# Kernel optimization log

Measured on AMD Instinct MI355X. Metric: run time of the kernel, lower is better.

## Reference

```python
import jax, jax.numpy as jnp
import numpy as np

D_MODEL = 1024
NUM_HEADS = 16
HEAD_DIM = D_MODEL // NUM_HEADS


def setup_inputs() -> dict:
    key = jax.random.key(0)
    k1, k2, k3 = jax.random.split(key, 3)
    B, S = 4, 2048
    x = jax.random.normal(k1, (B, S, D_MODEL), dtype=jnp.float32)
    # Linear weights; scale like torch's default-ish init for numerical sanity.
    w_qkv = jax.random.normal(k2, (D_MODEL, 3 * D_MODEL), dtype=jnp.float32) / np.sqrt(D_MODEL)
    b_qkv = jnp.zeros((3 * D_MODEL,), dtype=jnp.float32)
    w_out = jax.random.normal(k3, (D_MODEL, D_MODEL), dtype=jnp.float32) / np.sqrt(D_MODEL)
    b_out = jnp.zeros((D_MODEL,), dtype=jnp.float32)
    return {"x": x, "w_qkv": w_qkv, "b_qkv": b_qkv, "w_out": w_out, "b_out": b_out}


def reference(x, w_qkv, b_qkv, w_out, b_out):
    B, S, D = x.shape
    H, Hd = NUM_HEADS, HEAD_DIM
    # fused QKV projection, then chunk along last dim (same as torch.chunk)
    qkv = x @ w_qkv + b_qkv                       # [B, S, 3D]
    q, k, v = jnp.split(qkv, 3, axis=-1)          # each [B, S, D]
    q = q.reshape(B, S, H, Hd).transpose(0, 2, 1, 3)  # [B, H, S, Hd]
    k = k.reshape(B, S, H, Hd).transpose(0, 2, 1, 3)
    v = v.reshape(B, S, H, Hd).transpose(0, 2, 1, 3)
    scale = 1.0 / np.sqrt(Hd).astype(np.float32)
    scores = jnp.einsum('bhqd,bhkd->bhqk', q, k) * scale  # [B, H, S, S]
    attn = jax.nn.softmax(scores, axis=-1)
    out = jnp.einsum('bhqk,bhkd->bhqd', attn, v)           # [B, H, S, Hd]
    out = out.transpose(0, 2, 1, 3).reshape(B, S, D)
    return out @ w_out + b_out
```

## Files before the change

kernel.cpp:

```cpp
#include <hip/hip_runtime.h>
#include <stdint.h>

typedef unsigned short u16;
typedef __attribute__((ext_vector_type(8))) short   short8;
typedef __attribute__((ext_vector_type(8))) u16     ushort8;
typedef __attribute__((ext_vector_type(4))) float   f32x4;
typedef __attribute__((ext_vector_type(16))) float  f32x16;
typedef __attribute__((ext_vector_type(4))) unsigned int u32x4;

#define SEQ   2048
#define NH    16
#define HD    64
#define DM    1024
#define ROWS  8192
#define BHN   64

__device__ __forceinline__ u16 f2bf(float f){
  union { float f; uint32_t u; } v; v.f = f;
  return (u16)((v.u + 0x7fffu + ((v.u >> 16) & 1u)) >> 16);
}

__device__ __forceinline__ unsigned cvtpk(float a, float b){
  unsigned r;
  asm("v_cvt_pk_bf16_f32 %0, %1, %2" : "=v"(r) : "v"(a), "v"(b));
  return r;
}

__device__ __forceinline__ void pswap(unsigned &a, unsigned &b){
  asm volatile("v_permlane32_swap_b32 %0, %1" : "+v"(a), "+v"(b));
}

__device__ __forceinline__ float fexp2(float x){
  return __builtin_amdgcn_exp2f(x);
}

__device__ __forceinline__ float tsum16(const f32x16& s){
  float a0=s[0]+s[1], a1=s[2]+s[3], a2=s[4]+s[5], a3=s[6]+s[7];
  float a4=s[8]+s[9], a5=s[10]+s[11], a6=s[12]+s[13], a7=s[14]+s[15];
  float b0=a0+a1, b1=a2+a3, b2=a4+a5, b3=a6+a7;
  return (b0+b1)+(b2+b3);
}

#define GAS(p) ((const __attribute__((address_space(1))) void*)(p))
#define LAS(p) ((__attribute__((address_space(3))) void*)(p))

__global__ void conv_bf16_kernel(const float* __restrict__ in, u16* __restrict__ out, int n8){
  int i = blockIdx.x * blockDim.x + threadIdx.x;
  if (i >= n8) return;
  const float4* p = (const float4*)in + (size_t)i * 2;
  float4 a = p[0], b = p[1];
  ushort8 o;
  o[0]=f2bf(a.x); o[1]=f2bf(a.y); o[2]=f2bf(a.z); o[3]=f2bf(a.w);
  o[4]=f2bf(b.x); o[5]=f2bf(b.y); o[6]=f2bf(b.z); o[7]=f2bf(b.w);
  *(ushort8*)(out + (size_t)i * 8) = o;
}

__global__ void transpose_conv_kernel(const float* __restrict__ in, u16* __restrict__ out,
                                      int R, int C){
  __shared__ float tile[32][33];
  int c0 = blockIdx.x * 32, r0 = blockIdx.y * 32;
  int tx = threadIdx.x & 31, ty = threadIdx.x >> 5;
  #pragma unroll
  for (int i = 0; i < 4; i++)
    tile[ty + 8*i][tx] = in[(size_t)(r0 + ty + 8*i) * C + c0 + tx];
  __syncthreads();
  #pragma unroll
  for (int i = 0; i < 4; i++)
    out[(size_t)(c0 + ty + 8*i) * R + r0 + tx] = f2bf(tile[tx][ty + 8*i]);
}

#define BM 128
#define BN 128
#define BK 64

template<int MODE>
__global__ __launch_bounds__(256, 2) void gemm_kernel(
    const u16* __restrict__ A, const u16* __restrict__ Bt, const float* __restrict__ bias,
    u16* __restrict__ Qo, u16* __restrict__ Ko, u16* __restrict__ Vto,
    float* __restrict__ Cout)
{
  __shared__ __align__(16) u16 As[BM * BK];
  __shared__ __align__(16) u16 Bs[BN * BK];
  const int tid  = threadIdx.x;
  const int lane = tid & 63, wv = tid >> 6;
  const int wr = wv >> 1, wc = wv & 1;
  const int m0 = blockIdx.y * BM, n0 = blockIdx.x * BN;
  const int K = 1024;

  f32x4 acc[4][4] = {};

  for (int k0 = 0; k0 < K; k0 += BK) {
    #pragma unroll
    for (int i = 0; i < 4; i++) {
      int f = (i * 256 + tid) * 16;
      int row = f >> 7, inrow = f & 127;
      int src = inrow ^ ((row & 7) << 4);
      const u16* ga = A  + (size_t)(m0 + row) * K + k0 + (src >> 1);
      __builtin_amdgcn_global_load_lds(GAS(ga), LAS((char*)As + (i*256 + (wv<<6))*16), 16, 0, 0);
      const u16* gb = Bt + (size_t)(n0 + row) * K + k0 + (src >> 1);
      __builtin_amdgcn_global_load_lds(GAS(gb), LAS((char*)Bs + (i*256 + (wv<<6))*16), 16, 0, 0);
    }
    __syncthreads();
    #pragma unroll
    for (int kk = 0; kk < 2; kk++) {
      short8 af[4], bfr[4];
      #pragma unroll
      for (int i = 0; i < 4; i++) {
        int row = wr*64 + i*16 + (lane & 15);
        int kb  = (kk*64 + 16*(lane >> 4)) ^ ((row & 7) << 4);
        af[i] = *(const short8*)((const char*)As + row*128 + kb);
      }
      #pragma unroll
      for (int j = 0; j < 4; j++) {
        int row = wc*64 + j*16 + (lane & 15);
        int kb  = (kk*64 + 16*(lane >> 4)) ^ ((row & 7) << 4);
        bfr[j] = *(const short8*)((const char*)Bs + row*128 + kb);
      }
      #pragma unroll
      for (int i = 0; i < 4; i++)
        #pragma unroll
        for (int j = 0; j < 4; j++)
          acc[i][j] = __builtin_amdgcn_mfma_f32_16x16x32_bf16(af[i], bfr[j], acc[i][j], 0, 0, 0);
    }
    __syncthreads();
  }

  if (MODE == 0) {
    const int part = n0 >> 10;
    #pragma unroll
    for (int i = 0; i < 4; i++) {
      int row = m0 + wr*64 + i*16 + ((lane >> 4) << 2);
      int b = row >> 11, s = row & 2047;
      #pragma unroll
      for (int j = 0; j < 4; j++) {
        int col = n0 + wc*64 + j*16 + (lane & 15);
        int cn = col & 1023, h = cn >> 6, d = cn & 63;
        int bh = b * NH + h;
        #pragma unroll
        for (int r = 0; r < 4; r++) {
          float v = acc[i][j][r] + bias[col];
          int ss = s + r;
          if (part == 0)      Qo [((size_t)bh*SEQ + ss)*HD + d] = f2bf(v * 0.18033688011f);
          else if (part == 1) Ko [((size_t)bh*SEQ + ss)*HD + d] = f2bf(v);
          else                Vto[((size_t)bh*HD  + d)*SEQ + ss] = f2bf(v);
        }
      }
    }
  } else {
    #pragma unroll
    for (int i = 0; i < 4; i++) {
      int row = m0 + wr*64 + i*16 + ((lane >> 4) << 2);
      #pragma unroll
      for (int j = 0; j < 4; j++) {
        int col = n0 + wc*64 + j*16 + (lane & 15);
        float bv = bias[col];
        #pragma unroll
        for (int r = 0; r < 4; r++)
          Cout[(size_t)(row + r) * DM + col] = acc[i][j][r] + bv;
      }
    }
  }
}

#define STAGE(LOFF, T) do { \
    _Pragma("unroll") \
    for (int _i = 0; _i < 2; _i++) { \
      int _row = _i * 32 + (tid >> 3); \
      int _src = (((tid & 7) << 4) ^ ((_row & 7) << 4)) >> 1; \
      const u16* _gk = Kg + (((size_t)bh * SEQ + (T) * 64 + _row) << 6) + _src; \
      __builtin_amdgcn_global_load_lds(GAS(_gk), LAS(lds + (LOFF) + _i * 4096 + (wv << 10)), 16, 0, 0); \
      const u16* _gv = Vt + ((size_t)(bh * 64 + _row)) * SEQ + (T) * 64 + _src; \
      __builtin_amdgcn_global_load_lds(GAS(_gv), LAS(lds + (LOFF) + 8192 + _i * 4096 + (wv << 10)), 16, 0, 0); \
    } \
  } while (0)

#define WAITBAR() do { \
    asm volatile("s_waitcnt vmcnt(0) lgkmcnt(0)" ::: "memory"); \
    __builtin_amdgcn_s_barrier(); \
  } while (0)

#define PACK_PA(S, PA0, PA1) do { \
    unsigned a0 = cvtpk((S)[0],  (S)[1]),  b0 = cvtpk((S)[4],  (S)[5]); \
    unsigned a1 = cvtpk((S)[2],  (S)[3]),  b1 = cvtpk((S)[6],  (S)[7]); \
    unsigned a2 = cvtpk((S)[8],  (S)[9]),  b2 = cvtpk((S)[12], (S)[13]); \
    unsigned a3 = cvtpk((S)[10], (S)[11]), b3 = cvtpk((S)[14], (S)[15]); \
    pswap(a0, b0); pswap(a1, b1); pswap(a2, b2); pswap(a3, b3); \
    (PA0).u = (u32x4){a0, a1, b0, b1}; \
    (PA1).u = (u32x4){a2, a3, b2, b3}; \
  } while (0)

#define TILE64(BOFF) do { \
    _Pragma("unroll") \
    for (int H = 0; H < 2; H++) { \
      short8 kf[4]; \
      _Pragma("unroll") \
      for (int kd = 0; kd < 4; kd++) \
        kf[kd] = *(const short8*)(lds + (BOFF) + (32*H + l31) * 128 + ((32*kd + 16*hi) ^ swz)); \
      f32x16 sA, sB; \
      _Pragma("unroll") for (int i = 0; i < 16; i++) { sA[i] = -16.f; sB[i] = -16.f; } \
      __builtin_amdgcn_s_setprio(1); \
      _Pragma("unroll") \
      for (int kd = 0; kd < 4; kd++) { \
        sA = __builtin_amdgcn_mfma_f32_32x32x16_bf16(kf[kd], qfA[kd], sA, 0, 0, 0); \
        sB = __builtin_amdgcn_mfma_f32_32x32x16_bf16(kf[kd], qfB[kd], sB, 0, 0, 0); \
      } \
      __builtin_amdgcn_s_setprio(0); \
      _Pragma("unroll") for (int i = 0; i < 16; i++) { sA[i] = fexp2(sA[i]); sB[i] = fexp2(sB[i]); } \
      lpA += tsum16(sA); lpB += tsum16(sB); \
      union { u32x4 u; short8 s8; } paA0, paA1, paB0, paB1; \
      PACK_PA(sA, paA0, paA1); \
      PACK_PA(sB, paB0, paB1); \
      __builtin_amdgcn_s_setprio(1); \
      _Pragma("unroll") \
      for (int ki = 0; ki < 2; ki++) { \
        int vo = (64*H + 32*ki + 16*hi) ^ swz; \
        short8 vb0 = *(const short8*)(lds + (BOFF) + 8192  + l31 * 128 + vo); \
        short8 vb1 = *(const short8*)(lds + (BOFF) + 12288 + l31 * 128 + vo); \
        const short8 pA = ki ? paA1.s8 : paA0.s8; \
        const short8 pB = ki ? paB1.s8 : paB0.s8; \
        oA0 = __builtin_amdgcn_mfma_f32_32x32x16_bf16(pA, vb0, oA0, 0, 0, 0); \
        oA1 = __builtin_amdgcn_mfma_f32_32x32x16_bf16(pA, vb1, oA1, 0, 0, 0); \
        oB0 = __builtin_amdgcn_mfma_f32_32x32x16_bf16(pB, vb0, oB0, 0, 0, 0); \
        oB1 = __builtin_amdgcn_mfma_f32_32x32x16_bf16(pB, vb1, oB1, 0, 0, 0); \
      } \
      __builtin_amdgcn_s_setprio(0); \
    } \
  } while (0)

__global__ __launch_bounds__(256, 2) void attn_kernel(
    const u16* __restrict__ Q, const u16* __restrict__ Kg,
    const u16* __restrict__ Vt, u16* __restrict__ O)
{
  __shared__ __align__(16) char lds[32768];
  const int tid = threadIdx.x, lane = tid & 63, wv = tid >> 6;
  const int l31 = lane & 31, hi = lane >> 5;
  const int swz = (lane & 7) << 4;

  int flat = blockIdx.x;
  int nid = (flat & 7) * 64 + (flat >> 3);
  int bh = nid >> 3;
  int q0 = (nid & 7) * 256;

  short8 qfA[4], qfB[4];
  {
    int qrow = q0 + wv * 64 + l31;
    const u16* qp = Q + (((size_t)bh * SEQ + qrow) << 6) + hi * 8;
    #pragma unroll
    for (int kd = 0; kd < 4; kd++) {
      qfA[kd] = *(const short8*)(qp + kd * 16);
      qfB[kd] = *(const short8*)(qp + 2048 + kd * 16);
    }
  }

  f32x16 oA0 = {}, oA1 = {}, oB0 = {}, oB1 = {};
  float lpA = 0.f, lpB = 0.f;

  STAGE(0, 0);
  WAITBAR();
  for (int t = 0; t < 32; t += 2) {
    STAGE(16384, t + 1);
    TILE64(0);
    WAITBAR();
    if (t + 2 < 32) STAGE(0, t + 2);
    TILE64(16384);
    WAITBAR();
  }

  float lfA = lpA + __shfl_xor(lpA, 32);
  float lfB = lpB + __shfl_xor(lpB, 32);
  int b = bh >> 4, h = bh & 15;
  int qbase = q0 + wv * 64;
  #pragma unroll
  for (int r = 0; r < 16; r++) {
    int qrow = (r & 3) + 8 * (r >> 2) + 4 * hi;
    float invA = 1.0f / __shfl(lfA, qrow);
    float invB = 1.0f / __shfl(lfB, qrow);
    size_t rowA = ((size_t)(b * SEQ + qbase + qrow) << 10) + h * 64 + l31;
    size_t rowB = rowA + (32u << 10);
    O[rowA]      = f2bf(oA0[r] * invA);
    O[rowA + 32] = f2bf(oA1[r] * invA);
    O[rowB]      = f2bf(oB0[r] * invB);
    O[rowB + 32] = f2bf(oB1[r] * invB);
  }
}

extern "C" void kernel_launch(void* const* d_in, const int* in_sizes, int n_in,
                              void* d_out, int out_size, void* d_ws, size_t ws_size,
                              hipStream_t stream)
{
  const float* x     = (const float*)d_in[0];
  const float* w_qkv = (const float*)d_in[1];
  const float* b_qkv = (const float*)d_in[2];
  const float* w_out = (const float*)d_in[3];
  const float* b_out = (const float*)d_in[4];
  float* out = (float*)d_out;

  char* w = (char*)d_ws;
  u16* xb    = (u16*)(w);
  u16* wqkvT = (u16*)(w + 16777216);
  u16* woutT = (u16*)(w + 23068672);
  u16* Qw    = (u16*)(w + 25165824);
  u16* Kw    = (u16*)(w + 41943040);
  u16* Vtw   = (u16*)(w + 58720256);
  u16* Ow    = (u16*)(w + 75497472);

  conv_bf16_kernel<<<dim3(4096), dim3(256), 0, stream>>>(x, xb, ROWS * DM / 8);
  transpose_conv_kernel<<<dim3(96, 32), dim3(256), 0, stream>>>(w_qkv, wqkvT, 1024, 3072);
  transpose_conv_kernel<<<dim3(32, 32), dim3(256), 0, stream>>>(w_out, woutT, 1024, 1024);

  gemm_kernel<0><<<dim3(24, 64), dim3(256), 0, stream>>>(xb, wqkvT, b_qkv, Qw, Kw, Vtw, nullptr);
  attn_kernel<<<dim3(512), dim3(256), 0, stream>>>(Qw, Kw, Vtw, Ow);
  gemm_kernel<1><<<dim3(8, 64), dim3(256), 0, stream>>>(Ow, woutT, b_out, nullptr, nullptr, nullptr, out);
}
```

Before: 194.8 us.

## Replace QKV projection GEMM with 256x256 double-buffered 8-wave pipelined kernel

Adds a new QKV projection GEMM that uses 256x256 tiles, 8 waves per block and 128KB of double-buffered LDS. Async global-to-LDS loads of later K tiles are interleaved with MFMA sub-blocks, with partial vmcnt waits, s_setprio around the MFMAs, and an XCD-aware block remapping. The aim is better data reuse and hiding of load latency in the largest GEMM. The cost is heavy LDS use that limits occupancy, many barriers, and a more fragile hand-written schedule. The output projection GEMM is de-templated and otherwise unchanged.

```diff
diff --git a/kernel.cpp b/kernel.cpp
--- a/kernel.cpp
+++ b/kernel.cpp
@@ -43,6 +43,10 @@
 
 #define GAS(p) ((const __attribute__((address_space(1))) void*)(p))
 #define LAS(p) ((__attribute__((address_space(3))) void*)(p))
+
+#define BAR()   asm volatile("s_barrier" ::: "memory")
+#define BARV6() asm volatile("s_waitcnt vmcnt(6)\n\ts_barrier" ::: "memory")
+#define BARV0() asm volatile("s_waitcnt vmcnt(0)\n\ts_barrier" ::: "memory")
 
 __global__ void conv_bf16_kernel(const float* __restrict__ in, u16* __restrict__ out, int n8){
   int i = blockIdx.x * blockDim.x + threadIdx.x;
@@ -69,14 +73,146 @@
     out[(size_t)(c0 + ty + 8*i) * R + r0 + tx] = f2bf(tile[tx][ty + 8*i]);
 }
 
+__global__ __launch_bounds__(512, 2) void gemm8_kernel(
+    const u16* __restrict__ A, const u16* __restrict__ Bt, const float* __restrict__ bias,
+    u16* __restrict__ Qo, u16* __restrict__ Ko, u16* __restrict__ Vto)
+{
+  __shared__ __align__(16) char lds[131072];
+  const int tid = threadIdx.x, lane = tid & 63, wv = tid >> 6;
+  const int wm = wv >> 2, wn = wv & 3;
+  const int l15 = lane & 15, l4 = lane >> 4;
+
+  int bid = blockIdx.x;
+  int nid = (bid & 7) * 48 + (bid >> 3);
+  int tm = nid / 12, tn = nid - tm * 12;
+  const int m0 = tm * 256, n0 = tn * 256;
+
+  f32x4 acc[8][4] = {};
+
+  #define STG(REGION, SRC, ROW0, KT) do { \
+    _Pragma("unroll") \
+    for (int _u = 0; _u < 2; _u++) { \
+      int _r = _u*64 + (tid >> 3); \
+      int _sb = ((((tid & 7) << 4) ^ ((_r & 7) << 4)) >> 1); \
+      const u16* _g = (SRC) + (((size_t)((ROW0) + _r)) << 10) + ((KT) << 6) + _sb; \
+      __builtin_amdgcn_global_load_lds(GAS(_g), LAS(lds + (REGION) + _u*8192 + (wv << 10)), 16, 0, 0); \
+    } \
+  } while (0)
+
+  STG(0,              A,  m0,       0);
+  STG(16384,          A,  m0 + 128, 0);
+  STG(32768,          Bt, n0,       0);
+  STG(49152,          Bt, n0 + 128, 0);
+  STG(65536 + 49152,  Bt, n0 + 128, 1);
+  STG(65536 + 32768,  Bt, n0,       1);
+  STG(65536 + 16384,  A,  m0 + 128, 1);
+  BARV6();
+
+  short8 Af[4][2], Bf[2][2][2];
+
+  #define LD_A(BUF, M) do { \
+    _Pragma("unroll") for (int mr = 0; mr < 4; mr++) \
+      _Pragma("unroll") for (int kk = 0; kk < 2; kk++) { \
+        int row = (M)*64 + mr*16 + l15; \
+        Af[mr][kk] = *(const short8*)(lds + (BUF)*65536 + wm*16384 + row*128 \
+                       + ((kk*64 + 16*l4) ^ ((row & 7) << 4))); \
+      } \
+  } while (0)
+
+  #define LD_B(BUF, N) do { \
+    _Pragma("unroll") for (int jr = 0; jr < 2; jr++) \
+      _Pragma("unroll") for (int kk = 0; kk < 2; kk++) { \
+        int row = (wn & 1)*64 + (N)*32 + jr*16 + l15; \
+        Bf[N][jr][kk] = *(const short8*)(lds + (BUF)*65536 + 32768 + (wn >> 1)*16384 + row*128 \
+                          + ((kk*64 + 16*l4) ^ ((row & 7) << 4))); \
+      } \
+  } while (0)
+
+  #define MM(M, N) do { \
+    __builtin_amdgcn_s_setprio(1); \
+    _Pragma("unroll") for (int mr = 0; mr < 4; mr++) \
+      _Pragma("unroll") for (int jr = 0; jr < 2; jr++) \
+        _Pragma("unroll") for (int kk = 0; kk < 2; kk++) \
+          acc[(M)*4 + mr][(N)*2 + jr] = __builtin_amdgcn_mfma_f32_16x16x32_bf16( \
+              Af[mr][kk], Bf[N][jr][kk], acc[(M)*4 + mr][(N)*2 + jr], 0, 0, 0); \
+    __builtin_amdgcn_s_setprio(0); \
+  } while (0)
+
+  for (int i = 0; i < 7; i++) {
+    int t1 = 2*i + 1, t2 = 2*i + 2, t3 = 2*i + 3;
+    LD_A(0, 0); LD_B(0, 0);
+    STG(65536 + 0, A, m0, t1);
+    BAR();  MM(0, 0);  BAR();
+    LD_B(0, 1);
+    BAR();  MM(0, 1);  BAR();
+    LD_A(0, 1);
+    STG(32768, Bt, n0, t2);
+    STG(49152, Bt, n0 + 128, t2);
+    BAR();  MM(1, 1);  BAR();
+    STG(16384, A, m0 + 128, t2);
+    BAR();  MM(1, 0);  BARV6();
+    LD_A(1, 0); LD_B(1, 0);
+    STG(0, A, m0, t2);
+    BAR();  MM(0, 0);  BAR();
+    LD_B(1, 1);
+    BAR();  MM(0, 1);  BAR();
+    LD_A(1, 1);
+    STG(65536 + 32768, Bt, n0, t3);
+    STG(65536 + 49152, Bt, n0 + 128, t3);
+    BAR();  MM(1, 1);  BAR();
+    STG(65536 + 16384, A, m0 + 128, t3);
+    BAR();  MM(1, 0);  BARV6();
+  }
+
+  LD_A(0, 0); LD_B(0, 0);
+  STG(65536 + 0, A, m0, 15);
+  BAR();  MM(0, 0);  BAR();
+  LD_B(0, 1);
+  BAR();  MM(0, 1);  BAR();
+  LD_A(0, 1);
+  BAR();  MM(1, 1);  BAR();
+  BAR();  MM(1, 0);  BARV0();
+  LD_A(1, 0); LD_B(1, 0);
+  BAR();  MM(0, 0);  BAR();
+  LD_B(1, 1);
+  BAR();  MM(0, 1);  BAR();
+  LD_A(1, 1);
+  BAR();  MM(1, 1);  BAR();
+  MM(1, 0);
+
+  #undef STG
+  #undef LD_A
+  #undef LD_B
+  #undef MM
+
+  const int part = n0 >> 10;
+  #pragma unroll
+  for (int i = 0; i < 8; i++) {
+    int row = m0 + wm*128 + i*16 + (l4 << 2);
+    int b = row >> 11, s = row & 2047;
+    #pragma unroll
+    for (int j = 0; j < 4; j++) {
+      int col = n0 + wn*64 + j*16 + l15;
+      int cn = col & 1023, h = cn >> 6, d = cn & 63;
+      int bh = b * NH + h;
+      #pragma unroll
+      for (int r = 0; r < 4; r++) {
+        float v = acc[i][j][r] + bias[col];
+        int ss = s + r;
+        if (part == 0)      Qo [((size_t)bh*SEQ + ss)*HD + d] = f2bf(v * 0.18033688011f);
+        else if (part == 1) Ko [((size_t)bh*SEQ + ss)*HD + d] = f2bf(v);
+        else                Vto[((size_t)bh*HD  + d)*SEQ + ss] = f2bf(v);
+      }
+    }
+  }
+}
+
 #define BM 128
 #define BN 128
 #define BK 64
 
-template<int MODE>
 __global__ __launch_bounds__(256, 2) void gemm_kernel(
     const u16* __restrict__ A, const u16* __restrict__ Bt, const float* __restrict__ bias,
-    u16* __restrict__ Qo, u16* __restrict__ Ko, u16* __restrict__ Vto,
     float* __restrict__ Cout)
 {
   __shared__ __align__(16) u16 As[BM * BK];
@@ -125,39 +261,16 @@
     __syncthreads();
   }
 
-  if (MODE == 0) {
-    const int part = n0 >> 10;
+  #pragma unroll
+  for (int i = 0; i < 4; i++) {
+    int row = m0 + wr*64 + i*16 + ((lane >> 4) << 2);
     #pragma unroll
-    for (int i = 0; i < 4; i++) {
-      int row = m0 + wr*64 + i*16 + ((lane >> 4) << 2);
-      int b = row >> 11, s = row & 2047;
+    for (int j = 0; j < 4; j++) {
+      int col = n0 + wc*64 + j*16 + (lane & 15);
+      float bv = bias[col];
       #pragma unroll
-      for (int j = 0; j < 4; j++) {
-        int col = n0 + wc*64 + j*16 + (lane & 15);
-        int cn = col & 1023, h = cn >> 6, d = cn & 63;
-        int bh = b * NH + h;
-        #pragma unroll
-        for (int r = 0; r < 4; r++) {
-          float v = acc[i][j][r] + bias[col];
-          int ss = s + r;
-          if (part == 0)      Qo [((size_t)bh*SEQ + ss)*HD + d] = f2bf(v * 0.18033688011f);
-          else if (part == 1) Ko [((size_t)bh*SEQ + ss)*HD + d] = f2bf(v);
-          else                Vto[((size_t)bh*HD  + d)*SEQ + ss] = f2bf(v);
-        }
-      }
-    }
-  } else {
-    #pragma unroll
-    for (int i = 0; i < 4; i++) {
-      int row = m0 + wr*64 + i*16 + ((lane >> 4) << 2);
-      #pragma unroll
-      for (int j = 0; j < 4; j++) {
-        int col = n0 + wc*64 + j*16 + (lane & 15);
-        float bv = bias[col];
-        #pragma unroll
-        for (int r = 0; r < 4; r++)
-          Cout[(size_t)(row + r) * DM + col] = acc[i][j][r] + bv;
-      }
+      for (int r = 0; r < 4; r++)
+        Cout[(size_t)(row + r) * DM + col] = acc[i][j][r] + bv;
     }
   }
 }
@@ -175,8 +288,7 @@
   } while (0)
 
 #define WAITBAR() do { \
-    asm volatile("s_waitcnt vmcnt(0) lgkmcnt(0)" ::: "memory"); \
-    __builtin_amdgcn_s_barrier(); \
+    asm volatile("s_waitcnt vmcnt(0) lgkmcnt(0)\n\ts_barrier" ::: "memory"); \
   } while (0)
 
 #define PACK_PA(S, PA0, PA1) do { \
@@ -308,7 +420,7 @@
   transpose_conv_kernel<<<dim3(96, 32), dim3(256), 0, stream>>>(w_qkv, wqkvT, 1024, 3072);
   transpose_conv_kernel<<<dim3(32, 32), dim3(256), 0, stream>>>(w_out, woutT, 1024, 1024);
 
-  gemm_kernel<0><<<dim3(24, 64), dim3(256), 0, stream>>>(xb, wqkvT, b_qkv, Qw, Kw, Vtw, nullptr);
+  gemm8_kernel<<<dim3(384), dim3(512), 0, stream>>>(xb, wqkvT, b_qkv, Qw, Kw, Vtw);
   attn_kernel<<<dim3(512), dim3(256), 0, stream>>>(Qw, Kw, Vtw, Ow);
-  gemm_kernel<1><<<dim3(8, 64), dim3(256), 0, stream>>>(Ow, woutT, b_out, nullptr, nullptr, nullptr, out);
-}
+  gemm_kernel<<<dim3(8, 64), dim3(256), 0, stream>>>(Ow, woutT, b_out, out);
+}
```

New measurement: 203.4 us. +4.4%, slower.

## Halve attention query tile per block to double grid and occupancy

Applied to the files above, without the earlier changes.

The attention kernel now gives each wave 32 query rows instead of 64, so each block covers 128 queries and the grid grows from 512 to 1024 blocks. Launch bounds go from 2 to 4 blocks per CU, since the per-wave accumulator count halves. This is meant to fill the 256 CUs better and hide latency through higher occupancy. The cost is that every K/V tile is loaded into LDS twice as often per query, which doubles global and LDS traffic per unit of compute. The wait-and-barrier pair is also merged into a single inline asm block.

```diff
diff --git a/kernel.cpp b/kernel.cpp
--- a/kernel.cpp
+++ b/kernel.cpp
@@ -175,8 +175,7 @@
   } while (0)
 
 #define WAITBAR() do { \
-    asm volatile("s_waitcnt vmcnt(0) lgkmcnt(0)" ::: "memory"); \
-    __builtin_amdgcn_s_barrier(); \
+    asm volatile("s_waitcnt vmcnt(0) lgkmcnt(0)\n\ts_barrier" ::: "memory"); \
   } while (0)
 
 #define PACK_PA(S, PA0, PA1) do { \
@@ -196,38 +195,32 @@
       _Pragma("unroll") \
       for (int kd = 0; kd < 4; kd++) \
         kf[kd] = *(const short8*)(lds + (BOFF) + (32*H + l31) * 128 + ((32*kd + 16*hi) ^ swz)); \
-      f32x16 sA, sB; \
-      _Pragma("unroll") for (int i = 0; i < 16; i++) { sA[i] = -16.f; sB[i] = -16.f; } \
+      f32x16 s; \
+      _Pragma("unroll") for (int i = 0; i < 16; i++) s[i] = -16.f; \
       __builtin_amdgcn_s_setprio(1); \
       _Pragma("unroll") \
-      for (int kd = 0; kd < 4; kd++) { \
-        sA = __builtin_amdgcn_mfma_f32_32x32x16_bf16(kf[kd], qfA[kd], sA, 0, 0, 0); \
-        sB = __builtin_amdgcn_mfma_f32_32x32x16_bf16(kf[kd], qfB[kd], sB, 0, 0, 0); \
-      } \
+      for (int kd = 0; kd < 4; kd++) \
+        s = __builtin_amdgcn_mfma_f32_32x32x16_bf16(kf[kd], qf[kd], s, 0, 0, 0); \
       __builtin_amdgcn_s_setprio(0); \
-      _Pragma("unroll") for (int i = 0; i < 16; i++) { sA[i] = fexp2(sA[i]); sB[i] = fexp2(sB[i]); } \
-      lpA += tsum16(sA); lpB += tsum16(sB); \
-      union { u32x4 u; short8 s8; } paA0, paA1, paB0, paB1; \
-      PACK_PA(sA, paA0, paA1); \
-      PACK_PA(sB, paB0, paB1); \
+      _Pragma("unroll") for (int i = 0; i < 16; i++) s[i] = fexp2(s[i]); \
+      lp += tsum16(s); \
+      union { u32x4 u; short8 s8; } pa0, pa1; \
+      PACK_PA(s, pa0, pa1); \
       __builtin_amdgcn_s_setprio(1); \
       _Pragma("unroll") \
       for (int ki = 0; ki < 2; ki++) { \
         int vo = (64*H + 32*ki + 16*hi) ^ swz; \
-        short8 vb0 = *(const short8*)(lds + (BOFF) + 8192  + l31 * 128 + vo); \
-        short8 vb1 = *(const short8*)(lds + (BOFF) + 12288 + l31 * 128 + vo); \
-        const short8 pA = ki ? paA1.s8 : paA0.s8; \
-        const short8 pB = ki ? paB1.s8 : paB0.s8; \
-        oA0 = __builtin_amdgcn_mfma_f32_32x32x16_bf16(pA, vb0, oA0, 0, 0, 0); \
-        oA1 = __builtin_amdgcn_mfma_f32_32x32x16_bf16(pA, vb1, oA1, 0, 0, 0); \
-        oB0 = __builtin_amdgcn_mfma_f32_32x32x16_bf16(pB, vb0, oB0, 0, 0, 0); \
-        oB1 = __builtin_amdgcn_mfma_f32_32x32x16_bf16(pB, vb1, oB1, 0, 0, 0); \
+        short8 vb0 = *(const short8*)(lds + (BOFF) + 8192 + l31 * 128 + vo);             \
+        short8 vb1 = *(const short8*)(lds + (BOFF) + 8192 + (32 + l31) * 128 + vo);      \
+        const short8 pa = ki ? pa1.s8 : pa0.s8; \
+        oacc0 = __builtin_amdgcn_mfma_f32_32x32x16_bf16(pa, vb0, oacc0, 0, 0, 0); \
+        oacc1 = __builtin_amdgcn_mfma_f32_32x32x16_bf16(pa, vb1, oacc1, 0, 0, 0); \
       } \
       __builtin_amdgcn_s_setprio(0); \
     } \
   } while (0)
 
-__global__ __launch_bounds__(256, 2) void attn_kernel(
+__global__ __launch_bounds__(256, 4) void attn_kernel(
     const u16* __restrict__ Q, const u16* __restrict__ Kg,
     const u16* __restrict__ Vt, u16* __restrict__ O)
 {
@@ -237,23 +230,20 @@
   const int swz = (lane & 7) << 4;
 
   int flat = blockIdx.x;
-  int nid = (flat & 7) * 64 + (flat >> 3);
-  int bh = nid >> 3;
-  int q0 = (nid & 7) * 256;
-
-  short8 qfA[4], qfB[4];
+  int nid = (flat & 7) * 128 + (flat >> 3);
+  int bh = nid >> 4;
+  int q0 = (nid & 15) * 128;
+
+  short8 qf[4];
   {
-    int qrow = q0 + wv * 64 + l31;
+    int qrow = q0 + wv * 32 + l31;
     const u16* qp = Q + (((size_t)bh * SEQ + qrow) << 6) + hi * 8;
     #pragma unroll
-    for (int kd = 0; kd < 4; kd++) {
-      qfA[kd] = *(const short8*)(qp + kd * 16);
-      qfB[kd] = *(const short8*)(qp + 2048 + kd * 16);
-    }
-  }
-
-  f32x16 oA0 = {}, oA1 = {}, oB0 = {}, oB1 = {};
-  float lpA = 0.f, lpB = 0.f;
+    for (int kd = 0; kd < 4; kd++) qf[kd] = *(const short8*)(qp + kd * 16);
+  }
+
+  f32x16 oacc0 = {}, oacc1 = {};
+  float lp = 0.f;
 
   STAGE(0, 0);
   WAITBAR();
@@ -266,21 +256,16 @@
     WAITBAR();
   }
 
-  float lfA = lpA + __shfl_xor(lpA, 32);
-  float lfB = lpB + __shfl_xor(lpB, 32);
+  float lfull = lp + __shfl_xor(lp, 32);
   int b = bh >> 4, h = bh & 15;
-  int qbase = q0 + wv * 64;
+  int qbase = q0 + wv * 32;
   #pragma unroll
   for (int r = 0; r < 16; r++) {
     int qrow = (r & 3) + 8 * (r >> 2) + 4 * hi;
-    float invA = 1.0f / __shfl(lfA, qrow);
-    float invB = 1.0f / __shfl(lfB, qrow);
-    size_t rowA = ((size_t)(b * SEQ + qbase + qrow) << 10) + h * 64 + l31;
-    size_t rowB = rowA + (32u << 10);
-    O[rowA]      = f2bf(oA0[r] * invA);
-    O[rowA + 32] = f2bf(oA1[r] * invA);
-    O[rowB]      = f2bf(oB0[r] * invB);
-    O[rowB + 32] = f2bf(oB1[r] * invB);
+    float inv = 1.0f / __shfl(lfull, qrow);
+    size_t rowb = ((size_t)(b * SEQ + qbase + qrow) << 10) + h * 64 + l31;
+    O[rowb]      = f2bf(oacc0[r] * inv);
+    O[rowb + 32] = f2bf(oacc1[r] * inv);
   }
 }
 
@@ -309,6 +294,6 @@
   transpose_conv_kernel<<<dim3(32, 32), dim3(256), 0, stream>>>(w_out, woutT, 1024, 1024);
 
   gemm_kernel<0><<<dim3(24, 64), dim3(256), 0, stream>>>(xb, wqkvT, b_qkv, Qw, Kw, Vtw, nullptr);
-  attn_kernel<<<dim3(512), dim3(256), 0, stream>>>(Qw, Kw, Vtw, Ow);
+  attn_kernel<<<dim3(1024), dim3(256), 0, stream>>>(Qw, Kw, Vtw, Ow);
   gemm_kernel<1><<<dim3(8, 64), dim3(256), 0, stream>>>(Ow, woutT, b_out, nullptr, nullptr, nullptr, out);
 }
```

Result: slower. 391.3 us (+100.9%).

## Merge prep kernels into one launch and double attention K/V staging depth

Applied to the files above, without the earlier changes.

Merges the x conversion and the two weight transpose-convert kernels into a single prep_kernel that dispatches on block index, removing two launches. In attention, the LDS buffer grows to 64KB so each stage loads two 64-key tiles, and each barrier now covers two tiles of compute instead of one. This halves the barriers per KV sweep but doubles LDS per block, which can reduce occupancy and leaves more prefetch latency exposed per stage.

```diff
diff --git a/kernel.cpp b/kernel.cpp
--- a/kernel.cpp
+++ b/kernel.cpp
@@ -44,22 +44,27 @@
 #define GAS(p) ((const __attribute__((address_space(1))) void*)(p))
 #define LAS(p) ((__attribute__((address_space(3))) void*)(p))
 
-__global__ void conv_bf16_kernel(const float* __restrict__ in, u16* __restrict__ out, int n8){
-  int i = blockIdx.x * blockDim.x + threadIdx.x;
-  if (i >= n8) return;
-  const float4* p = (const float4*)in + (size_t)i * 2;
-  float4 a = p[0], b = p[1];
-  ushort8 o;
-  o[0]=f2bf(a.x); o[1]=f2bf(a.y); o[2]=f2bf(a.z); o[3]=f2bf(a.w);
-  o[4]=f2bf(b.x); o[5]=f2bf(b.y); o[6]=f2bf(b.z); o[7]=f2bf(b.w);
-  *(ushort8*)(out + (size_t)i * 8) = o;
-}
-
-__global__ void transpose_conv_kernel(const float* __restrict__ in, u16* __restrict__ out,
-                                      int R, int C){
+__global__ void prep_kernel(const float* __restrict__ x, u16* __restrict__ xb,
+                            const float* __restrict__ wqkv, u16* __restrict__ wqkvT,
+                            const float* __restrict__ wout, u16* __restrict__ woutT)
+{
   __shared__ float tile[32][33];
-  int c0 = blockIdx.x * 32, r0 = blockIdx.y * 32;
-  int tx = threadIdx.x & 31, ty = threadIdx.x >> 5;
+  const int bid = blockIdx.x, tid = threadIdx.x;
+  if (bid < 4096) {
+    int i = bid * 256 + tid;
+    const float4* p = (const float4*)x + (size_t)i * 2;
+    float4 a = p[0], b = p[1];
+    ushort8 o;
+    o[0]=f2bf(a.x); o[1]=f2bf(a.y); o[2]=f2bf(a.z); o[3]=f2bf(a.w);
+    o[4]=f2bf(b.x); o[5]=f2bf(b.y); o[6]=f2bf(b.z); o[7]=f2bf(b.w);
+    *(ushort8*)(xb + (size_t)i * 8) = o;
+    return;
+  }
+  const float* in; u16* out; int R, C, bx, by;
+  if (bid < 7168) { in = wqkv; out = wqkvT; R = 1024; C = 3072; int b2 = bid - 4096; bx = b2 % 96; by = b2 / 96; }
+  else            { in = wout; out = woutT; R = 1024; C = 1024; int b2 = bid - 7168; bx = b2 % 32; by = b2 / 32; }
+  int c0 = bx * 32, r0 = by * 32;
+  int tx = tid & 31, ty = tid >> 5;
   #pragma unroll
   for (int i = 0; i < 4; i++)
     tile[ty + 8*i][tx] = in[(size_t)(r0 + ty + 8*i) * C + c0 + tx];
@@ -174,9 +179,10 @@
     } \
   } while (0)
 
+#define STAGE2(LOFF, T) do { STAGE(LOFF, T); STAGE((LOFF) + 16384, (T) + 1); } while (0)
+
 #define WAITBAR() do { \
-    asm volatile("s_waitcnt vmcnt(0) lgkmcnt(0)" ::: "memory"); \
-    __builtin_amdgcn_s_barrier(); \
+    asm volatile("s_waitcnt vmcnt(0) lgkmcnt(0)\n\ts_barrier" ::: "memory"); \
   } while (0)
 
 #define PACK_PA(S, PA0, PA1) do { \
@@ -214,7 +220,7 @@
       _Pragma("unroll") \
       for (int ki = 0; ki < 2; ki++) { \
         int vo = (64*H + 32*ki + 16*hi) ^ swz; \
-        short8 vb0 = *(const short8*)(lds + (BOFF) + 8192  + l31 * 128 + vo); \
+        short8 vb0 = *(const short8*)(lds + (BOFF) + 8192 + l31 * 128 + vo); \
         short8 vb1 = *(const short8*)(lds + (BOFF) + 12288 + l31 * 128 + vo); \
         const short8 pA = ki ? paA1.s8 : paA0.s8; \
         const short8 pB = ki ? paB1.s8 : paB0.s8; \
@@ -231,7 +237,7 @@
     const u16* __restrict__ Q, const u16* __restrict__ Kg,
     const u16* __restrict__ Vt, u16* __restrict__ O)
 {
-  __shared__ __align__(16) char lds[32768];
+  __shared__ __align__(16) char lds[65536];
   const int tid = threadIdx.x, lane = tid & 63, wv = tid >> 6;
   const int l31 = lane & 31, hi = lane >> 5;
   const int swz = (lane & 7) << 4;
@@ -255,14 +261,16 @@
   f32x16 oA0 = {}, oA1 = {}, oB0 = {}, oB1 = {};
   float lpA = 0.f, lpB = 0.f;
 
-  STAGE(0, 0);
+  STAGE2(0, 0);
   WAITBAR();
-  for (int t = 0; t < 32; t += 2) {
-    STAGE(16384, t + 1);
+  for (int t = 0; t < 32; t += 4) {
+    STAGE2(32768, t + 2);
     TILE64(0);
+    TILE64(16384);
     WAITBAR();
-    if (t + 2 < 32) STAGE(0, t + 2);
-    TILE64(16384);
+    if (t + 4 < 32) STAGE2(0, t + 4);
+    TILE64(32768);
+    TILE64(49152);
     WAITBAR();
   }
 
@@ -304,10 +312,7 @@
   u16* Vtw   = (u16*)(w + 58720256);
   u16* Ow    = (u16*)(w + 75497472);
 
-  conv_bf16_kernel<<<dim3(4096), dim3(256), 0, stream>>>(x, xb, ROWS * DM / 8);
-  transpose_conv_kernel<<<dim3(96, 32), dim3(256), 0, stream>>>(w_qkv, wqkvT, 1024, 3072);
-  transpose_conv_kernel<<<dim3(32, 32), dim3(256), 0, stream>>>(w_out, woutT, 1024, 1024);
-
+  prep_kernel<<<dim3(8192), dim3(256), 0, stream>>>(x, xb, w_qkv, wqkvT, w_out, woutT);
   gemm_kernel<0><<<dim3(24, 64), dim3(256), 0, stream>>>(xb, wqkvT, b_qkv, Qw, Kw, Vtw, nullptr);
   attn_kernel<<<dim3(512), dim3(256), 0, stream>>>(Qw, Kw, Vtw, Ow);
   gemm_kernel<1><<<dim3(8, 64), dim3(256), 0, stream>>>(Ow, woutT, b_out, nullptr, nullptr, nullptr, out);
```

Measured after the change: 244.6 us. 1.26x slower.
